# Kernel optimization log

Hardware: AMD Instinct MI355X
Metric: run time of the kernel (lower is better)

## Reference

```python
import jax, jax.numpy as jnp
import numpy as np

B, H, S, D = 1, 16, 4096, 64

def setup_inputs() -> dict:
    key = jax.random.key(0)
    kq, kk, kv = jax.random.split(key, 3)
    return {
        "query": jax.random.normal(kq, (B, H, S, D), dtype=jnp.float32),
        "key": jax.random.normal(kk, (B, H, S, D), dtype=jnp.float32),
        "value": jax.random.normal(kv, (B, H, S, D), dtype=jnp.float32),
    }

def reference(query, key, value):
    # qk: [B,H,S,S] materialized score matrix (unfused, as in original)
    qk = jnp.einsum("bhqd,bhkd->bhqk", query, key)
    attn = jax.nn.softmax(qk, axis=-1)
    # dropout_p = 0.0 -> identity
    out = jnp.einsum("bhqk,bhkd->bhqd", attn, value)
    return out
```

## Files before the change

### kernel.cpp

```cpp
#include <hip/hip_runtime.h>
#include <math.h>


#define HH 16
#define SS 4096
#define DDm 64
#define KB 64
#define NTL (SS / KB)
#define LDP 72

typedef __attribute__((ext_vector_type(2))) _Float16 half2_t;
typedef __attribute__((ext_vector_type(8))) _Float16 half8_t;
typedef __attribute__((ext_vector_type(16))) float f32x16;

union H8 { half2_t h2[4]; half8_t v; };
union FU { float f; unsigned u; };
union HU { half2_t h; unsigned u; };

__device__ inline unsigned asu(float x){ FU c; c.f=x; return c.u; }
__device__ inline float    asf(unsigned x){ FU c; c.u=x; return c.f; }
__device__ inline unsigned h2u(half2_t x){ HU c; c.h=x; return c.u; }
__device__ inline half2_t  u2h(unsigned x){ HU c; c.u=x; return c.h; }
__device__ inline half2_t  pk2(float a, float b){ half2_t h; h[0]=(_Float16)a; h[1]=(_Float16)b; return h; }

#if __has_builtin(__builtin_amdgcn_permlane32_swap)
#define HAVE_PL32 1
typedef __attribute__((ext_vector_type(2))) unsigned uint2_t;
__device__ inline uint2_t pl32(unsigned a, unsigned b){
  return __builtin_amdgcn_permlane32_swap(a, b, false, false);
}
#endif

#if __has_builtin(__builtin_amdgcn_exp2f)
#define EXP2F(x) __builtin_amdgcn_exp2f(x)
#else
#define EXP2F(x) exp2f(x)
#endif
#define L2E 1.44269504088896f

__global__ __launch_bounds__(256)
void prepack(const float* __restrict__ K, const float* __restrict__ V,
             _Float16* __restrict__ Kh, _Float16* __restrict__ Vth) {
  const int g = blockIdx.x;
  const int tid = threadIdx.x;
  if (g < 2048) {
    const int gt = g * 256 + tid;
    const int dg = gt & 7, r = (gt >> 3) & 63, t = (gt >> 9) & 63, h = gt >> 15;
    const float* src = K + ((size_t)(h * SS + t * 64 + r)) * DDm + dg * 8;
    float4 a = *(const float4*)src;
    float4 b = *(const float4*)(src + 4);
    H8 w;
    w.h2[0] = pk2(a.x, a.y); w.h2[1] = pk2(a.z, a.w);
    w.h2[2] = pk2(b.x, b.y); w.h2[3] = pk2(b.z, b.w);
    *(half8_t*)(Kh + (size_t)(h * 64 + t) * 4096 + (dg * 64 + r) * 8) = w.v;
  } else {
    const int gt = (g - 2048) * 256 + tid;
    const int dr = gt & 63, kg = (gt >> 6) & 7, t = (gt >> 9) & 63, h = gt >> 15;
    const float* src = V + ((size_t)(h * SS + t * 64 + kg * 8)) * DDm + dr;
    H8 w;
#pragma unroll
    for (int j = 0; j < 4; ++j)
      w.h2[j] = pk2(src[(2 * j) * DDm], src[(2 * j + 1) * DDm]);
    *(half8_t*)(Vth + (size_t)(h * 64 + t) * 4096 + (kg * 64 + dr) * 8) = w.v;
  }
}

__global__ __launch_bounds__(256, 2)
void attn_main(const float* __restrict__ Q, const _Float16* __restrict__ Kh,
               const _Float16* __restrict__ Vth, float* __restrict__ O) {
  const int tid  = threadIdx.x;
  const int lane = tid & 63;
  const int lo5  = lane & 31;
  const int hi   = lane >> 5;
  const int wv   = tid >> 6;

  const int lid  = blockIdx.x;
  const int head = 2 * (lid & 7) + ((lid >> 3) & 1);
  const int qt   = lid >> 4;
  const int qbase = qt * 128 + wv * 32;
  const size_t hoff = (size_t)head * SS * DDm;

  H8 qf[4];
  {
    const float* qp = Q + hoff + (size_t)(qbase + lo5) * DDm;
#pragma unroll
    for (int ds = 0; ds < 4; ++ds) {
      float4 a = *(const float4*)(qp + 16 * ds + 8 * hi);
      float4 b = *(const float4*)(qp + 16 * ds + 8 * hi + 4);
      qf[ds].h2[0] = pk2(a.x, a.y); qf[ds].h2[1] = pk2(a.z, a.w);
      qf[ds].h2[2] = pk2(b.x, b.y); qf[ds].h2[3] = pk2(b.z, b.w);
    }
  }

  const _Float16* ktb = Kh + (size_t)head * 64 * 4096 + (hi * 64 + lo5) * 8;
  const _Float16* vtb = Vth + (size_t)head * 64 * 4096 + (hi * 64 + lo5) * 8;

  auto loadK = [&](int t, half8_t (&k)[8]) {
    const _Float16* p = ktb + (size_t)t * 4096;
#pragma unroll
    for (int s = 0; s < 2; ++s)
#pragma unroll
      for (int ds = 0; ds < 4; ++ds)
        k[s * 4 + ds] = *(const half8_t*)(p + (ds * 128 + 32 * s) * 8);
  };
  auto loadV = [&](int t, half8_t (&v)[8]) {
    const _Float16* p = vtb + (size_t)t * 4096;
#pragma unroll
    for (int s = 0; s < 2; ++s)
#pragma unroll
      for (int sp = 0; sp < 2; ++sp)
#pragma unroll
        for (int nt = 0; nt < 2; ++nt)
          v[s * 4 + sp * 2 + nt] = *(const half8_t*)(p + ((s * 2 + sp) * 128 + nt * 32) * 8);
  };

  f32x16 acc[2];
#pragma unroll
  for (int nt = 0; nt < 2; ++nt)
#pragma unroll
    for (int r = 0; r < 16; ++r) acc[nt][r] = 0.f;
  float m_run = -INFINITY, l_run = 0.f;

  auto compute = [&](half8_t (&k)[8], half8_t (&v)[8]) {
#pragma unroll
    for (int s = 0; s < 2; ++s) {
      f32x16 st;
#pragma unroll
      for (int r = 0; r < 16; ++r) st[r] = 0.f;
#pragma unroll
      for (int ds = 0; ds < 4; ++ds)
        st = __builtin_amdgcn_mfma_f32_32x32x16_f16(k[s * 4 + ds], qf[ds].v, st, 0, 0, 0);

      float a0 = fmaxf(st[0], st[1]),   a1 = fmaxf(st[2], st[3]);
      float a2 = fmaxf(st[4], st[5]),   a3 = fmaxf(st[6], st[7]);
      float a4 = fmaxf(st[8], st[9]),   a5 = fmaxf(st[10], st[11]);
      float a6 = fmaxf(st[12], st[13]), a7 = fmaxf(st[14], st[15]);
      float b0 = fmaxf(a0, a1), b1 = fmaxf(a2, a3);
      float b2 = fmaxf(a4, a5), b3 = fmaxf(a6, a7);
      float tmax = fmaxf(fmaxf(b0, b1), fmaxf(b2, b3));
#if HAVE_PL32
      { uint2_t pr = pl32(asu(tmax), asu(tmax)); tmax = fmaxf(asf(pr[0]), asf(pr[1])); }
#else
      tmax = fmaxf(tmax, __shfl_xor(tmax, 32, 64));
#endif
      if (__any(tmax > m_run + 8.f)) {
        float mnew = fmaxf(m_run, tmax);
        float corr = EXP2F((m_run - mnew) * L2E);
        m_run = mnew; l_run *= corr;
#pragma unroll
        for (int r = 0; r < 16; ++r) {
          const int qr = (r & 3) + 8 * (r >> 2) + 4 * hi;
          float cf = asf(__builtin_amdgcn_ds_bpermute(qr << 2, asu(corr)));
          acc[0][r] *= cf; acc[1][r] *= cf;
        }
      }

      const float mt = m_run * L2E;
      float p[16];
      float s0 = 0.f, s1 = 0.f, s2 = 0.f, s3 = 0.f;
#pragma unroll
      for (int r = 0; r < 16; r += 4) {
        p[r]     = EXP2F(__builtin_fmaf(st[r],     L2E, -mt)); s0 += p[r];
        p[r + 1] = EXP2F(__builtin_fmaf(st[r + 1], L2E, -mt)); s1 += p[r + 1];
        p[r + 2] = EXP2F(__builtin_fmaf(st[r + 2], L2E, -mt)); s2 += p[r + 2];
        p[r + 3] = EXP2F(__builtin_fmaf(st[r + 3], L2E, -mt)); s3 += p[r + 3];
      }
      float lsum = (s0 + s1) + (s2 + s3);
#if HAVE_PL32
      { uint2_t pr = pl32(asu(lsum), asu(lsum)); lsum = asf(pr[0]) + asf(pr[1]); }
#else
      lsum += __shfl_xor(lsum, 32, 64);
#endif
      l_run += lsum;

      H8 pa[2];
#pragma unroll
      for (int step = 0; step < 2; ++step) {
        const int b = 8 * step;
        half2_t x0 = pk2(p[b + 0], p[b + 1]);
        half2_t x1 = pk2(p[b + 2], p[b + 3]);
        half2_t y0 = pk2(p[b + 4], p[b + 5]);
        half2_t y1 = pk2(p[b + 6], p[b + 7]);
#if HAVE_PL32
        uint2_t sA = pl32(h2u(x0), h2u(y0));
        uint2_t sB = pl32(h2u(x1), h2u(y1));
        pa[step].h2[0] = u2h(sA[0]); pa[step].h2[1] = u2h(sB[0]);
        pa[step].h2[2] = u2h(sA[1]); pa[step].h2[3] = u2h(sB[1]);
#else
        half2_t sx0 = u2h(__shfl_xor(h2u(x0), 32, 64));
        half2_t sx1 = u2h(__shfl_xor(h2u(x1), 32, 64));
        half2_t sy0 = u2h(__shfl_xor(h2u(y0), 32, 64));
        half2_t sy1 = u2h(__shfl_xor(h2u(y1), 32, 64));
        pa[step].h2[0] = hi ? sy0 : x0;  pa[step].h2[1] = hi ? sy1 : x1;
        pa[step].h2[2] = hi ? y0 : sx0;  pa[step].h2[3] = hi ? y1 : sx1;
#endif
      }
#pragma unroll
      for (int step = 0; step < 2; ++step)
#pragma unroll
        for (int nt = 0; nt < 2; ++nt)
          acc[nt] = __builtin_amdgcn_mfma_f32_32x32x16_f16(pa[step].v, v[s * 4 + step * 2 + nt], acc[nt], 0, 0, 0);
    }
  };

  half8_t kA[8], vA[8], kB[8], vB[8];
  loadK(0, kA); loadV(0, vA);
  for (int t = 0; t < NTL; t += 2) {
    loadK(t + 1, kB); loadV(t + 1, vB);
    compute(kA, vA);
    if (t + 2 < NTL) { loadK(t + 2, kA); loadV(t + 2, vA); }
    compute(kB, vB);
  }

  const float invl = 1.f / l_run;
#pragma unroll
  for (int r = 0; r < 16; ++r) {
    const int qr = (r & 3) + 8 * (r >> 2) + 4 * hi;
    float il = asf(__builtin_amdgcn_ds_bpermute(qr << 2, asu(invl)));
    float* op = O + hoff + (size_t)(qbase + qr) * DDm + lo5;
    op[0]  = acc[0][r] * il;
    op[32] = acc[1][r] * il;
  }
}

__global__ __launch_bounds__(512, 2)
void attn_fwd_fb(const float* __restrict__ Q, const float* __restrict__ K,
                 const float* __restrict__ V, float* __restrict__ O) {
  __shared__ __align__(16) _Float16 Klds[2][KB][LDP];
  __shared__ __align__(16) _Float16 Vt  [2][DDm][LDP];

  const int tid  = threadIdx.x;
  const int lane = tid & 63;
  const int lo5  = lane & 31;
  const int hi   = lane >> 5;

  const int lid  = blockIdx.x;
  const int head = 2 * (lid & 7) + ((lid >> 3) & 1);
  const int qt   = lid >> 4;
  const int qbase = qt * 256 + (tid >> 6) * 32;
  const size_t hoff = (size_t)head * SS * DDm;

  H8 qf[4];
  {
    const float* qp = Q + hoff + (size_t)(qbase + lo5) * DDm;
#pragma unroll
    for (int ds = 0; ds < 4; ++ds) {
      float4 a = *(const float4*)(qp + 16 * ds + 8 * hi);
      float4 b = *(const float4*)(qp + 16 * ds + 8 * hi + 4);
      qf[ds].h2[0] = pk2(a.x, a.y); qf[ds].h2[1] = pk2(a.z, a.w);
      qf[ds].h2[2] = pk2(b.x, b.y); qf[ds].h2[3] = pk2(b.z, b.w);
    }
  }

  const int krow = tid >> 3, kc8 = (tid & 7) * 8;
  const int vd = tid & 63, vk8 = (tid >> 6) * 8;

  float4 ka, kb; float va[8];
  auto issue = [&](int t) {
    const float* kp = K + hoff + (size_t)(t * KB + krow) * DDm + kc8;
    ka = *(const float4*)kp;
    kb = *(const float4*)(kp + 4);
    const float* vp = V + hoff + (size_t)(t * KB + vk8) * DDm + vd;
#pragma unroll
    for (int j = 0; j < 8; ++j) va[j] = vp[j * DDm];
  };
  auto wstage = [&](int buf) {
    H8 kw;
    kw.h2[0] = pk2(ka.x, ka.y); kw.h2[1] = pk2(ka.z, ka.w);
    kw.h2[2] = pk2(kb.x, kb.y); kw.h2[3] = pk2(kb.z, kb.w);
    *(half8_t*)&Klds[buf][krow][kc8] = kw.v;
    H8 vw;
#pragma unroll
    for (int j = 0; j < 4; ++j) vw.h2[j] = pk2(va[2 * j], va[2 * j + 1]);
    *(half8_t*)&Vt[buf][vd][vk8] = vw.v;
  };

  f32x16 acc[2];
#pragma unroll
  for (int nt = 0; nt < 2; ++nt)
#pragma unroll
    for (int r = 0; r < 16; ++r) acc[nt][r] = 0.f;
  float m_run = -INFINITY, l_run = 0.f;

  issue(0); wstage(0); __syncthreads();

  for (int t = 0; t < NTL; ++t) {
    const int cur = t & 1;
    if (t + 1 < NTL) issue(t + 1);

#pragma unroll
    for (int s = 0; s < 2; ++s) {
      const int rs = 32 * s;
      f32x16 st;
#pragma unroll
      for (int r = 0; r < 16; ++r) st[r] = 0.f;
#pragma unroll
      for (int ds = 0; ds < 4; ++ds) {
        half8_t af = *(const half8_t*)&Klds[cur][rs + lo5][16 * ds + 8 * hi];
        st = __builtin_amdgcn_mfma_f32_32x32x16_f16(af, qf[ds].v, st, 0, 0, 0);
      }
      float tmax = st[0];
#pragma unroll
      for (int r = 1; r < 16; ++r) tmax = fmaxf(tmax, st[r]);
#if HAVE_PL32
      { uint2_t pr = pl32(asu(tmax), asu(tmax)); tmax = fmaxf(asf(pr[0]), asf(pr[1])); }
#else
      tmax = fmaxf(tmax, __shfl_xor(tmax, 32, 64));
#endif
      if (__any(tmax > m_run + 8.f)) {
        float mnew = fmaxf(m_run, tmax);
        float corr = __expf(m_run - mnew);
        m_run = mnew; l_run *= corr;
#pragma unroll
        for (int r = 0; r < 16; ++r) {
          const int qr = (r & 3) + 8 * (r >> 2) + 4 * hi;
          float cf = asf(__builtin_amdgcn_ds_bpermute(qr << 2, asu(corr)));
          acc[0][r] *= cf; acc[1][r] *= cf;
        }
      }
      float p[16]; float lsum = 0.f;
#pragma unroll
      for (int r = 0; r < 16; ++r) { p[r] = __expf(st[r] - m_run); lsum += p[r]; }
#if HAVE_PL32
      { uint2_t pr = pl32(asu(lsum), asu(lsum)); lsum = asf(pr[0]) + asf(pr[1]); }
#else
      lsum += __shfl_xor(lsum, 32, 64);
#endif
      l_run += lsum;
      H8 pa[2];
#pragma unroll
      for (int step = 0; step < 2; ++step) {
        const int b = 8 * step;
        half2_t x0 = pk2(p[b + 0], p[b + 1]);
        half2_t x1 = pk2(p[b + 2], p[b + 3]);
        half2_t y0 = pk2(p[b + 4], p[b + 5]);
        half2_t y1 = pk2(p[b + 6], p[b + 7]);
#if HAVE_PL32
        uint2_t sA = pl32(h2u(x0), h2u(y0));
        uint2_t sB = pl32(h2u(x1), h2u(y1));
        pa[step].h2[0] = u2h(sA[0]); pa[step].h2[1] = u2h(sB[0]);
        pa[step].h2[2] = u2h(sA[1]); pa[step].h2[3] = u2h(sB[1]);
#else
        half2_t sx0 = u2h(__shfl_xor(h2u(x0), 32, 64));
        half2_t sx1 = u2h(__shfl_xor(h2u(x1), 32, 64));
        half2_t sy0 = u2h(__shfl_xor(h2u(y0), 32, 64));
        half2_t sy1 = u2h(__shfl_xor(h2u(y1), 32, 64));
        pa[step].h2[0] = hi ? sy0 : x0;  pa[step].h2[1] = hi ? sy1 : x1;
        pa[step].h2[2] = hi ? y0 : sx0;  pa[step].h2[3] = hi ? y1 : sx1;
#endif
      }
#pragma unroll
      for (int step = 0; step < 2; ++step)
#pragma unroll
        for (int nt = 0; nt < 2; ++nt) {
          half8_t vb = *(const half8_t*)&Vt[cur][32 * nt + lo5][rs + 16 * step + 8 * hi];
          acc[nt] = __builtin_amdgcn_mfma_f32_32x32x16_f16(pa[step].v, vb, acc[nt], 0, 0, 0);
        }
    }

    __syncthreads();
    if (t + 1 < NTL) wstage((t + 1) & 1);
    __syncthreads();
  }

  const float invl = 1.f / l_run;
#pragma unroll
  for (int r = 0; r < 16; ++r) {
    const int qr = (r & 3) + 8 * (r >> 2) + 4 * hi;
    float il = asf(__builtin_amdgcn_ds_bpermute(qr << 2, asu(invl)));
    float* op = O + hoff + (size_t)(qbase + qr) * DDm + lo5;
    op[0]  = acc[0][r] * il;
    op[32] = acc[1][r] * il;
  }
}

extern "C" void kernel_launch(void* const* d_in, const int* in_sizes, int n_in,
                              void* d_out, int out_size, void* d_ws, size_t ws_size,
                              hipStream_t stream) {
  const float* Q = (const float*)d_in[0];
  const float* K = (const float*)d_in[1];
  const float* V = (const float*)d_in[2];
  float* O = (float*)d_out;
  const size_t need = (size_t)2 * HH * SS * DDm * sizeof(_Float16);
  if (ws_size >= need) {
    _Float16* Kh  = (_Float16*)d_ws;
    _Float16* Vth = Kh + (size_t)HH * SS * DDm;
    prepack<<<dim3(4096), dim3(256), 0, stream>>>(K, V, Kh, Vth);
    attn_main<<<dim3(512), dim3(256), 0, stream>>>(Q, Kh, Vth, O);
  } else {
    attn_fwd_fb<<<dim3(256), dim3(512), 0, stream>>>(Q, K, V, O);
  }
}
```

Measured before the change: 125.3 us.

## Split key range across wave pairs and merge partial softmax results via LDS

Each 32-query tile is now handled by two waves, each covering half of the key tiles, and their running max, sum and accumulators are merged through shared memory before writing the output. The grid doubles to 1024 blocks and the launch bound rises to 4 blocks per CU to raise occupancy and hide memory latency. In exchange it adds an LDS merge, a block barrier and extra rescaling work. The tighter register budget (double-buffered K/V fragments alone take many VGPRs) may force spills.

```diff
diff --git a/kernel.cpp b/kernel.cpp
--- a/kernel.cpp
+++ b/kernel.cpp
@@ -7,6 +7,7 @@
 #define DDm 64
 #define KB 64
 #define NTL (SS / KB)
+#define NTLH (NTL / 2)
 #define LDP 72
 
 typedef __attribute__((ext_vector_type(2))) _Float16 half2_t;
@@ -65,19 +66,25 @@
   }
 }
 
-__global__ __launch_bounds__(256, 2)
+__global__ __launch_bounds__(256, 4)
 void attn_main(const float* __restrict__ Q, const _Float16* __restrict__ Kh,
                const _Float16* __restrict__ Vth, float* __restrict__ O) {
+  __shared__ float AccL[2][32][64];
+  __shared__ float ML[2][2][32];
+  __shared__ float FL[2][2][32];
+
   const int tid  = threadIdx.x;
   const int lane = tid & 63;
   const int lo5  = lane & 31;
   const int hi   = lane >> 5;
   const int wv   = tid >> 6;
+  const int pair = wv >> 1;
+  const int half = wv & 1;
 
   const int lid  = blockIdx.x;
   const int head = 2 * (lid & 7) + ((lid >> 3) & 1);
   const int qt   = lid >> 4;
-  const int qbase = qt * 128 + wv * 32;
+  const int qbase = qt * 64 + pair * 32;
   const size_t hoff = (size_t)head * SS * DDm;
 
   H8 qf[4];
@@ -203,23 +210,40 @@
     }
   };
 
+  const int hb = half * NTLH;
   half8_t kA[8], vA[8], kB[8], vB[8];
-  loadK(0, kA); loadV(0, vA);
-  for (int t = 0; t < NTL; t += 2) {
-    loadK(t + 1, kB); loadV(t + 1, vB);
+  loadK(hb, kA); loadV(hb, vA);
+  for (int t = 0; t < NTLH; t += 2) {
+    loadK(hb + t + 1, kB); loadV(hb + t + 1, vB);
     compute(kA, vA);
-    if (t + 2 < NTL) { loadK(t + 2, kA); loadV(t + 2, vA); }
+    if (t + 2 < NTLH) { loadK(hb + t + 2, kA); loadV(hb + t + 2, vA); }
     compute(kB, vB);
   }
 
-  const float invl = 1.f / l_run;
-#pragma unroll
-  for (int r = 0; r < 16; ++r) {
-    const int qr = (r & 3) + 8 * (r >> 2) + 4 * hi;
-    float il = asf(__builtin_amdgcn_ds_bpermute(qr << 2, asu(invl)));
-    float* op = O + hoff + (size_t)(qbase + qr) * DDm + lo5;
-    op[0]  = acc[0][r] * il;
-    op[32] = acc[1][r] * il;
+  if (half == 1) {
+    if (hi == 0) { ML[pair][0][lo5] = m_run; ML[pair][1][lo5] = l_run; }
+#pragma unroll
+    for (int nt = 0; nt < 2; ++nt)
+#pragma unroll
+      for (int r = 0; r < 16; ++r) AccL[pair][nt * 16 + r][lane] = acc[nt][r];
+  }
+  __syncthreads();
+  if (half == 0) {
+    const float m1 = ML[pair][0][lo5], l1 = ML[pair][1][lo5];
+    const float m  = fmaxf(m_run, m1);
+    const float e0 = EXP2F((m_run - m) * L2E);
+    const float e1 = EXP2F((m1 - m) * L2E);
+    const float inv = 1.f / (l_run * e0 + l1 * e1);
+    if (hi == 0) { FL[pair][0][lo5] = e0 * inv; FL[pair][1][lo5] = e1 * inv; }
+#pragma unroll
+    for (int r = 0; r < 16; ++r) {
+      const int qr = (r & 3) + 8 * (r >> 2) + 4 * hi;
+      const float f0 = FL[pair][0][qr];
+      const float f1 = FL[pair][1][qr];
+      float* op = O + hoff + (size_t)(qbase + qr) * DDm + lo5;
+      op[0]  = acc[0][r] * f0 + AccL[pair][r][lane]      * f1;
+      op[32] = acc[1][r] * f0 + AccL[pair][16 + r][lane] * f1;
+    }
   }
 }
 
@@ -386,7 +410,7 @@
     _Float16* Kh  = (_Float16*)d_ws;
     _Float16* Vth = Kh + (size_t)HH * SS * DDm;
     prepack<<<dim3(4096), dim3(256), 0, stream>>>(K, V, Kh, Vth);
-    attn_main<<<dim3(512), dim3(256), 0, stream>>>(Q, Kh, Vth, O);
+    attn_main<<<dim3(1024), dim3(256), 0, stream>>>(Q, Kh, Vth, O);
   } else {
     attn_fwd_fb<<<dim3(256), dim3(512), 0, stream>>>(Q, K, V, O);
   }
```

Result: slower. 491.8 us (+292.4%).
